# Optimization experiments

Measured on AMD Instinct MI355X. Metric: run time of the kernel, lower is better.

## Reference

```python
import jax, jax.numpy as jnp
import numpy as np

TRANSLATE_STD = 0.125
SCALE_STD = 0.2
CUTOUT_SIZE = 0.5

B, C, H, W = 64, 3, 512, 512


def setup_inputs() -> dict:
    key = jax.random.key(0)
    ks = jax.random.split(key, 20)
    inp = {
        'images': jax.random.normal(ks[0], (B, C, H, W), dtype=jnp.float32),
        'u_angle': jax.random.uniform(ks[1], (B,), dtype=jnp.float32),
        'u_scale': jax.random.uniform(ks[2], (B,), dtype=jnp.float32),
        'u_trans': jax.random.uniform(ks[3], (B,), dtype=jnp.float32),
        'u_bright': jax.random.uniform(ks[4], (B,), dtype=jnp.float32),
        'u_contrast': jax.random.uniform(ks[5], (B,), dtype=jnp.float32),
        'u_sat': jax.random.uniform(ks[6], (B,), dtype=jnp.float32),
        'noise': jax.random.normal(ks[7], (B, C, H, W), dtype=jnp.float32),
        'm_flip': jax.random.randint(ks[8], (B,), 0, 2, dtype=jnp.int32),
        'm_rot': jax.random.randint(ks[9], (B,), 0, 2, dtype=jnp.int32),
        'm_scale': jax.random.randint(ks[10], (B,), 0, 2, dtype=jnp.int32),
        'm_trans': jax.random.randint(ks[11], (B,), 0, 2, dtype=jnp.int32),
        'm_bright': jax.random.randint(ks[12], (B,), 0, 2, dtype=jnp.int32),
        'm_contrast': jax.random.randint(ks[13], (B,), 0, 2, dtype=jnp.int32),
        'm_sat': jax.random.randint(ks[14], (B,), 0, 2, dtype=jnp.int32),
        'm_cut': jax.random.randint(ks[15], (B,), 0, 2, dtype=jnp.int32),
        'y0': jax.random.randint(ks[16], (B,), 0, H - int(H * CUTOUT_SIZE) + 1, dtype=jnp.int32),
        'x0': jax.random.randint(ks[17], (B,), 0, W - int(W * CUTOUT_SIZE) + 1, dtype=jnp.int32),
    }
    return inp


def _sample_bilinear_reflect(img, gx, gy):
    # img: [C,H,W]; gx, gy: [H,W] normalized coords in grid_sample convention
    # (align_corners=False, padding_mode='reflection')
    c, h, w = img.shape
    x = ((gx + 1.0) * w - 1.0) * 0.5
    y = ((gy + 1.0) * h - 1.0) * 0.5

    def reflect(v, size):
        # reflect about pixel edges [-0.5, size-0.5], then clip coordinate
        v = jnp.abs(v + 0.5)
        v = jnp.mod(v, 2.0 * size)
        v = jnp.minimum(v, 2.0 * size - v)
        return jnp.clip(v - 0.5, 0.0, size - 1.0)

    x = reflect(x, float(w))
    y = reflect(y, float(h))
    x0f = jnp.floor(x)
    y0f = jnp.floor(y)
    wx = x - x0f
    wy = y - y0f
    x0i = jnp.clip(x0f, 0, w - 1).astype(jnp.int32)
    x1i = jnp.clip(x0f + 1, 0, w - 1).astype(jnp.int32)
    y0i = jnp.clip(y0f, 0, h - 1).astype(jnp.int32)
    y1i = jnp.clip(y0f + 1, 0, h - 1).astype(jnp.int32)
    v00 = img[:, y0i, x0i]
    v01 = img[:, y0i, x1i]
    v10 = img[:, y1i, x0i]
    v11 = img[:, y1i, x1i]
    top = v00 + wx * (v01 - v00)
    bot = v10 + wx * (v11 - v10)
    return top + wy * (bot - top)


def reference(images, u_angle, u_scale, u_trans, u_bright, u_contrast, u_sat,
              noise, m_flip, m_rot, m_scale, m_trans, m_bright, m_contrast,
              m_sat, m_cut, y0, x0):
    b, c, h, w = images.shape
    # xflip
    images = jnp.where((m_flip > 0)[:, None, None, None], images[..., ::-1], images)
    # rotate / scale / translate (single value broadcast to both axes, as in original)
    angle = jnp.where(m_rot > 0, (u_angle * 2.0 - 1.0) * jnp.pi, 0.0)
    sc = jnp.where(m_scale > 0, (u_scale * 2.0 - 1.0) * SCALE_STD + 1.0, 1.0)
    tr = jnp.where(m_trans > 0, (u_trans * 2.0 - 1.0) * TRANSLATE_STD, 0.0)
    ca = jnp.cos(angle)[:, None, None]
    sa = jnp.sin(angle)[:, None, None]
    scb = sc[:, None, None]
    trb = tr[:, None, None]
    gx0, gy0 = jnp.meshgrid(jnp.linspace(-1.0, 1.0, w), jnp.linspace(-1.0, 1.0, h), indexing='xy')  # [H,W]
    gx = scb * (ca * gx0 - sa * gy0) + trb  # [B,H,W]
    gy = scb * (sa * gx0 + ca * gy0) + trb
    images = jax.vmap(_sample_bilinear_reflect)(images, gx, gy)
    # brightness
    bb = jnp.where(m_bright > 0, u_bright * 0.2, 0.0)
    images = jnp.clip(images + bb[:, None, None, None], -1.0, 1.0)
    # contrast
    cc = jnp.where(m_contrast > 0, u_contrast + 0.5, 1.0)
    images = jnp.clip(images * cc[:, None, None, None], -1.0, 1.0)
    # saturation: lerp(grayscale, images, s)
    ss = jnp.where(m_sat > 0, u_sat * 2.0, 1.0)[:, None, None, None]
    gray = images.mean(axis=1, keepdims=True)
    images = jnp.clip(gray + ss * (images - gray), -1.0, 1.0)
    ch, cw = int(h * CUTOUT_SIZE), int(w * CUTOUT_SIZE)
    ys = jnp.arange(h)[None, :, None]
    xs = jnp.arange(w)[None, None, :]
    y0b = y0[:, None, None]
    x0b = x0[:, None, None]
    cmask = (ys >= y0b) & (ys < y0b + ch) & (xs >= x0b) & (xs < x0b + cw)
    fmask = cmask & (m_cut > 0)[:, None, None]
    images = jnp.where(fmask[:, None, :, :], noise, images)
    return images
```

## Files before the change

kernel.cpp:

```cpp
#include <hip/hip_runtime.h>
#include <math.h>


constexpr int Bn = 64;
constexpr int Cn = 3;
constexpr int Hn = 512;
constexpr int Wn = 512;
constexpr float TRANSLATE_STD = 0.125f;
constexpr float SCALE_STD = 0.2f;
constexpr int CUT_H = 256;
constexpr int CUT_W = 256;

typedef float f2v __attribute__((ext_vector_type(2)));

__device__ __forceinline__ f2v load2(const float* p) {
    f2v r;
    __builtin_memcpy(&r, p, 8);
    return r;
}

__device__ __forceinline__ float reflect_coord(float v, float size) {
    v = fabsf(v + 0.5f);
    v = fmodf(v, 2.0f * size);
    v = fminf(v, 2.0f * size - v);
    return fminf(fmaxf(v - 0.5f, 0.0f), size - 1.0f);
}

__global__ __launch_bounds__(256) void augment_kernel(
    const float* __restrict__ images,
    const float* __restrict__ u_angle,
    const float* __restrict__ u_scale,
    const float* __restrict__ u_trans,
    const float* __restrict__ u_bright,
    const float* __restrict__ u_contrast,
    const float* __restrict__ u_sat,
    const float* __restrict__ noise,
    const int* __restrict__ m_flip,
    const int* __restrict__ m_rot,
    const int* __restrict__ m_scale,
    const int* __restrict__ m_trans,
    const int* __restrict__ m_bright,
    const int* __restrict__ m_contrast,
    const int* __restrict__ m_sat,
    const int* __restrict__ m_cut,
    const int* __restrict__ y0p,
    const int* __restrict__ x0p,
    float* __restrict__ out)
{
    const int x = blockIdx.x * 32 + threadIdx.x;
    const int y = blockIdx.y * 8 + threadIdx.y;
    const int b = blockIdx.z;

    const float angle = (m_rot[b] > 0) ? (u_angle[b] * 2.0f - 1.0f) * 3.14159265358979323846f : 0.0f;
    const float sc    = (m_scale[b] > 0) ? (u_scale[b] * 2.0f - 1.0f) * SCALE_STD + 1.0f : 1.0f;
    const float tr    = (m_trans[b] > 0) ? (u_trans[b] * 2.0f - 1.0f) * TRANSLATE_STD : 0.0f;
    const float bb    = (m_bright[b] > 0) ? u_bright[b] * 0.2f : 0.0f;
    const float cc    = (m_contrast[b] > 0) ? u_contrast[b] + 0.5f : 1.0f;
    const float ss    = (m_sat[b] > 0) ? u_sat[b] * 2.0f : 1.0f;
    const bool  flip  = m_flip[b] > 0;
    const bool  docut = m_cut[b] > 0;
    const int   cy0   = y0p[b];
    const int   cx0   = x0p[b];

    float saf, caf;
    __sincosf(angle, &saf, &caf);

    const float gx0 = -1.0f + (2.0f / 511.0f) * (float)x;
    const float gy0 = -1.0f + (2.0f / 511.0f) * (float)y;

    const float gx = sc * (caf * gx0 - saf * gy0) + tr;
    const float gy = sc * (saf * gx0 + caf * gy0) + tr;

    float xx = ((gx + 1.0f) * (float)Wn - 1.0f) * 0.5f;
    float yy = ((gy + 1.0f) * (float)Hn - 1.0f) * 0.5f;
    xx = reflect_coord(xx, (float)Wn);
    yy = reflect_coord(yy, (float)Hn);

    const float x0f = floorf(xx);
    const float y0f = floorf(yy);
    const float wx = xx - x0f;
    const float wy = yy - y0f;

    int x0i = (int)fminf(fmaxf(x0f, 0.0f), (float)(Wn - 1));
    int x1i = (int)fminf(x0f + 1.0f, (float)(Wn - 1));
    const int y0i = (int)fminf(fmaxf(y0f, 0.0f), (float)(Hn - 1));
    const int y1i = (int)fminf(y0f + 1.0f, (float)(Hn - 1));

    if (flip) { x0i = (Wn - 1) - x0i; x1i = (Wn - 1) - x1i; }

    const int xbase = min(min(x0i, x1i), Wn - 2);
    const bool s0 = (x0i != xbase);
    const bool s1 = (x1i != xbase);

    const size_t plane = (size_t)Hn * Wn;
    const float* imgb = images + (size_t)b * Cn * plane;
    const int r0 = y0i * Wn + xbase;
    const int r1 = y1i * Wn + xbase;

    float vals[Cn];
    #pragma unroll
    for (int c = 0; c < Cn; ++c) {
        const float* p = imgb + (size_t)c * plane;
        const f2v t0 = load2(p + r0);
        const f2v t1 = load2(p + r1);
        const float v00 = s0 ? t0.y : t0.x;
        const float v01 = s1 ? t0.y : t0.x;
        const float v10 = s0 ? t1.y : t1.x;
        const float v11 = s1 ? t1.y : t1.x;
        const float top = v00 + wx * (v01 - v00);
        const float bot = v10 + wx * (v11 - v10);
        float v = top + wy * (bot - top);
        v = fminf(fmaxf(v + bb, -1.0f), 1.0f);
        v = fminf(fmaxf(v * cc, -1.0f), 1.0f);
        vals[c] = v;
    }

    const float gray = (vals[0] + vals[1] + vals[2]) * (1.0f / 3.0f);
    const bool cut = docut && (y >= cy0) && (y < cy0 + CUT_H) && (x >= cx0) && (x < cx0 + CUT_W);

    const size_t base = (size_t)b * Cn * plane + (size_t)y * Wn + (size_t)x;
    #pragma unroll
    for (int c = 0; c < Cn; ++c) {
        float v = gray + ss * (vals[c] - gray);
        v = fminf(fmaxf(v, -1.0f), 1.0f);
        if (cut) v = __builtin_nontemporal_load(&noise[base + c * plane]);
        __builtin_nontemporal_store(v, &out[base + c * plane]);
    }
}

extern "C" void kernel_launch(void* const* d_in, const int* in_sizes, int n_in,
                              void* d_out, int out_size, void* d_ws, size_t ws_size,
                              hipStream_t stream) {
    const float* images     = (const float*)d_in[0];
    const float* u_angle    = (const float*)d_in[1];
    const float* u_scale    = (const float*)d_in[2];
    const float* u_trans    = (const float*)d_in[3];
    const float* u_bright   = (const float*)d_in[4];
    const float* u_contrast = (const float*)d_in[5];
    const float* u_sat      = (const float*)d_in[6];
    const float* noise      = (const float*)d_in[7];
    const int*   m_flip     = (const int*)d_in[8];
    const int*   m_rot      = (const int*)d_in[9];
    const int*   m_scale    = (const int*)d_in[10];
    const int*   m_trans    = (const int*)d_in[11];
    const int*   m_bright   = (const int*)d_in[12];
    const int*   m_contrast = (const int*)d_in[13];
    const int*   m_sat      = (const int*)d_in[14];
    const int*   m_cut      = (const int*)d_in[15];
    const int*   y0p        = (const int*)d_in[16];
    const int*   x0p        = (const int*)d_in[17];
    float* out = (float*)d_out;

    dim3 block(32, 8);
    dim3 grid(Wn / 32, Hn / 8, Bn);
    augment_kernel<<<grid, block, 0, stream>>>(
        images, u_angle, u_scale, u_trans, u_bright, u_contrast, u_sat, noise,
        m_flip, m_rot, m_scale, m_trans, m_bright, m_contrast, m_sat, m_cut,
        y0p, x0p, out);
}
```

Measured before the change: 511.4 us.

## Stage source footprint in LDS per 16x16 tile and loop tiles per block

Each block now handles eight 16x16 output tiles in sequence. For each tile it computes the bounding box of the rotated and scaled source footprint and loads that region into LDS with coalesced float4 loads, flipping in-register when needed. Bilinear taps then read from LDS instead of scattered 8-byte global loads. Tiles whose footprint nears an edge or is too tall (large scale or rotation) fall back to the original reflect path. Coordinates are stepped incrementally and clamps use fmed3. The cost is extra syncs and LDS traffic, plus divergence between the staged and fallback paths.

```diff
diff --git a/kernel.cpp b/kernel.cpp
--- a/kernel.cpp
+++ b/kernel.cpp
@@ -11,6 +11,14 @@
 constexpr int CUT_H = 256;
 constexpr int CUT_W = 256;
 
+constexpr int FW = 32;
+constexpr int FSTRIDE = 40;
+constexpr int FH_MAX = 32;
+constexpr int CH_LDS = FSTRIDE * FH_MAX;
+constexpr int NT = 8;
+constexpr uint32_t PLANE = 512u * 512u;
+
+typedef float f4v __attribute__((ext_vector_type(4)));
 typedef float f2v __attribute__((ext_vector_type(2)));
 
 __device__ __forceinline__ f2v load2(const float* p) {
@@ -47,9 +55,13 @@
     const int* __restrict__ x0p,
     float* __restrict__ out)
 {
-    const int x = blockIdx.x * 32 + threadIdx.x;
-    const int y = blockIdx.y * 8 + threadIdx.y;
-    const int b = blockIdx.z;
+    __shared__ __align__(16) float lds[Cn * CH_LDS];
+
+    const int tx  = threadIdx.x;
+    const int ty  = threadIdx.y;
+    const int sx0 = blockIdx.x * (16 * NT);
+    const int y   = blockIdx.y * 16 + ty;
+    const int b   = blockIdx.z;
 
     const float angle = (m_rot[b] > 0) ? (u_angle[b] * 2.0f - 1.0f) * 3.14159265358979323846f : 0.0f;
     const float sc    = (m_scale[b] > 0) ? (u_scale[b] * 2.0f - 1.0f) * SCALE_STD + 1.0f : 1.0f;
@@ -65,66 +77,142 @@
     float saf, caf;
     __sincosf(angle, &saf, &caf);
 
-    const float gx0 = -1.0f + (2.0f / 511.0f) * (float)x;
-    const float gy0 = -1.0f + (2.0f / 511.0f) * (float)y;
-
-    const float gx = sc * (caf * gx0 - saf * gy0) + tr;
-    const float gy = sc * (saf * gx0 + caf * gy0) + tr;
-
-    float xx = ((gx + 1.0f) * (float)Wn - 1.0f) * 0.5f;
-    float yy = ((gy + 1.0f) * (float)Hn - 1.0f) * 0.5f;
-    xx = reflect_coord(xx, (float)Wn);
-    yy = reflect_coord(yy, (float)Hn);
-
-    const float x0f = floorf(xx);
-    const float y0f = floorf(yy);
-    const float wx = xx - x0f;
-    const float wy = yy - y0f;
-
-    int x0i = (int)fminf(fmaxf(x0f, 0.0f), (float)(Wn - 1));
-    int x1i = (int)fminf(x0f + 1.0f, (float)(Wn - 1));
-    const int y0i = (int)fminf(fmaxf(y0f, 0.0f), (float)(Hn - 1));
-    const int y1i = (int)fminf(y0f + 1.0f, (float)(Hn - 1));
-
-    if (flip) { x0i = (Wn - 1) - x0i; x1i = (Wn - 1) - x1i; }
-
-    const int xbase = min(min(x0i, x1i), Wn - 2);
-    const bool s0 = (x0i != xbase);
-    const bool s1 = (x1i != xbase);
-
-    const size_t plane = (size_t)Hn * Wn;
-    const float* imgb = images + (size_t)b * Cn * plane;
-    const int r0 = y0i * Wn + xbase;
-    const int r1 = y1i * Wn + xbase;
-
-    float vals[Cn];
-    #pragma unroll
-    for (int c = 0; c < Cn; ++c) {
-        const float* p = imgb + (size_t)c * plane;
-        const f2v t0 = load2(p + r0);
-        const f2v t1 = load2(p + r1);
-        const float v00 = s0 ? t0.y : t0.x;
-        const float v01 = s1 ? t0.y : t0.x;
-        const float v10 = s0 ? t1.y : t1.x;
-        const float v11 = s1 ? t1.y : t1.x;
-        const float top = v00 + wx * (v01 - v00);
-        const float bot = v10 + wx * (v11 - v10);
-        float v = top + wy * (bot - top);
-        v = fminf(fmaxf(v + bb, -1.0f), 1.0f);
-        v = fminf(fmaxf(v * cc, -1.0f), 1.0f);
-        vals[c] = v;
-    }
-
-    const float gray = (vals[0] + vals[1] + vals[2]) * (1.0f / 3.0f);
-    const bool cut = docut && (y >= cy0) && (y < cy0 + CUT_H) && (x >= cx0) && (x < cx0 + CUT_W);
-
-    const size_t base = (size_t)b * Cn * plane + (size_t)y * Wn + (size_t)x;
-    #pragma unroll
-    for (int c = 0; c < Cn; ++c) {
-        float v = gray + ss * (vals[c] - gray);
-        v = fminf(fmaxf(v, -1.0f), 1.0f);
-        if (cut) v = __builtin_nontemporal_load(&noise[base + c * plane]);
-        __builtin_nontemporal_store(v, &out[base + c * plane]);
+    const float kk = sc * (512.0f / 511.0f);
+    const float dxdx = caf * kk, dxdy = -saf * kk;
+    const float dydx = saf * kk, dydy = caf * kk;
+    const float xx_org = 256.0f * (sc * (saf - caf) + tr + 1.0f) - 0.5f;
+    const float yy_org = 256.0f * (sc * (-saf - caf) + tr + 1.0f) - 0.5f;
+
+    const float step_x = 16.0f * dxdx;
+    const float step_y = 16.0f * dydx;
+
+    float xxt = xx_org + (float)(sx0 + tx) * dxdx + (float)y * dxdy;
+    float yyt = yy_org + (float)(sx0 + tx) * dydx + (float)y * dydy;
+
+    const float fty = (float)(blockIdx.y * 16);
+    float bx = xx_org + (float)sx0 * dxdx + fty * dxdy;
+    float by = yy_org + (float)sx0 * dydx + fty * dydy;
+    const float sxx = 15.0f * dxdx, sxy = 15.0f * dxdy;
+    const float syx = 15.0f * dydx, syy = 15.0f * dydy;
+    const float min_dx = fminf(sxx, 0.0f) + fminf(sxy, 0.0f);
+    const float max_dx = fmaxf(sxx, 0.0f) + fmaxf(sxy, 0.0f);
+    const float min_dy = fminf(syx, 0.0f) + fminf(syy, 0.0f);
+    const float max_dy = fmaxf(syx, 0.0f) + fmaxf(syy, 0.0f);
+
+    const float* __restrict__ imgb = images + (size_t)b * (Cn * PLANE);
+    float* __restrict__ outb       = out    + (size_t)b * (Cn * PLANE);
+    const float* __restrict__ noib = noise  + (size_t)b * (Cn * PLANE);
+
+    const int tid = ty * 16 + tx;
+    const int sr  = tid >> 3;
+    const int sq  = (tid & 7) << 2;
+
+    const bool ycut = docut && (y >= cy0) && (y < cy0 + CUT_H);
+    uint32_t opix = (uint32_t)y * 512u + (uint32_t)(sx0 + tx);
+
+    #pragma unroll 1
+    for (int t = 0; t < NT; ++t) {
+        const float minxx = bx + min_dx, maxxx = bx + max_dx;
+        const float minyy = by + min_dy, maxyy = by + max_dy;
+        bool cok = (minxx >= 1.0f) && (maxxx <= 509.0f) &&
+                   (minyy >= 1.0f) && (maxyy <= 509.0f);
+        int x_lo = 0, y_lo = 0, fh = 0;
+        if (cok) {
+            x_lo = min(((int)minxx - 1) & ~3, Wn - FW);
+            y_lo = (int)minyy - 1;
+            fh   = ((int)maxyy + 2) - y_lo + 1;
+            if (fh > FH_MAX) cok = false;
+        }
+
+        if (t > 0) __syncthreads();
+
+        if (cok && sr < fh) {
+            const int scol = flip ? (508 - x_lo - sq) : (x_lo + sq);
+            const uint32_t soff = (uint32_t)(y_lo + sr) * 512u + (uint32_t)scol;
+            f4v A = *(const f4v*)(imgb + soff);
+            f4v B = *(const f4v*)(imgb + soff + PLANE);
+            f4v C = *(const f4v*)(imgb + soff + 2 * PLANE);
+            if (flip) {
+                A = f4v{A.w, A.z, A.y, A.x};
+                B = f4v{B.w, B.z, B.y, B.x};
+                C = f4v{C.w, C.z, C.y, C.x};
+            }
+            float* d = &lds[sr * FSTRIDE + sq];
+            *(f4v*)(d)              = A;
+            *(f4v*)(d + CH_LDS)     = B;
+            *(f4v*)(d + 2 * CH_LDS) = C;
+        }
+        __syncthreads();
+
+        float vals[Cn];
+        if (cok) {
+            const float fx = xxt - (float)x_lo;
+            const float fy = yyt - (float)y_lo;
+            const int xi = (int)fx;
+            const int yi = (int)fy;
+            const float wx = fx - (float)xi;
+            const float wy = fy - (float)yi;
+            const float* ph = &lds[yi * FSTRIDE + xi];
+            #pragma unroll
+            for (int c = 0; c < Cn; ++c) {
+                const float v00 = ph[0], v01 = ph[1];
+                const float v10 = ph[FSTRIDE], v11 = ph[FSTRIDE + 1];
+                ph += CH_LDS;
+                const float top = v00 + wx * (v01 - v00);
+                const float bot = v10 + wx * (v11 - v10);
+                float v = top + wy * (bot - top);
+                v = __builtin_amdgcn_fmed3f(v + bb, -1.0f, 1.0f);
+                v = __builtin_amdgcn_fmed3f(v * cc, -1.0f, 1.0f);
+                vals[c] = v;
+            }
+        } else {
+            const float rxx = reflect_coord(xxt, (float)Wn);
+            const float ryy = reflect_coord(yyt, (float)Hn);
+            const float x0f = floorf(rxx);
+            const float y0f = floorf(ryy);
+            const float wx = rxx - x0f;
+            const float wy = ryy - y0f;
+            int x0i = (int)fminf(fmaxf(x0f, 0.0f), 511.0f);
+            int x1i = (int)fminf(x0f + 1.0f, 511.0f);
+            const int y0i = (int)fminf(fmaxf(y0f, 0.0f), 511.0f);
+            const int y1i = (int)fminf(y0f + 1.0f, 511.0f);
+            if (flip) { x0i = 511 - x0i; x1i = 511 - x1i; }
+            const int xbase = min(min(x0i, x1i), 510);
+            const bool s0 = (x0i != xbase);
+            const bool s1 = (x1i != xbase);
+            const uint32_t r0 = (uint32_t)(y0i * 512 + xbase);
+            const uint32_t r1 = (uint32_t)(y1i * 512 + xbase);
+            #pragma unroll
+            for (int c = 0; c < Cn; ++c) {
+                const f2v t0 = load2(imgb + r0 + c * PLANE);
+                const f2v t1 = load2(imgb + r1 + c * PLANE);
+                const float v00 = s0 ? t0.y : t0.x;
+                const float v01 = s1 ? t0.y : t0.x;
+                const float v10 = s0 ? t1.y : t1.x;
+                const float v11 = s1 ? t1.y : t1.x;
+                const float top = v00 + wx * (v01 - v00);
+                const float bot = v10 + wx * (v11 - v10);
+                float v = top + wy * (bot - top);
+                v = __builtin_amdgcn_fmed3f(v + bb, -1.0f, 1.0f);
+                v = __builtin_amdgcn_fmed3f(v * cc, -1.0f, 1.0f);
+                vals[c] = v;
+            }
+        }
+
+        const float gray = (vals[0] + vals[1] + vals[2]) * (1.0f / 3.0f);
+        const int xpix = sx0 + (t << 4) + tx;
+        const bool cut = ycut && (xpix >= cx0) && (xpix < cx0 + CUT_W);
+        #pragma unroll
+        for (int c = 0; c < Cn; ++c) {
+            float v = gray + ss * (vals[c] - gray);
+            v = __builtin_amdgcn_fmed3f(v, -1.0f, 1.0f);
+            if (cut) v = __builtin_nontemporal_load(&noib[opix + c * PLANE]);
+            __builtin_nontemporal_store(v, &outb[opix + c * PLANE]);
+        }
+
+        opix += 16;
+        bx += step_x; by += step_y;
+        xxt += step_x; yyt += step_y;
     }
 }
 
@@ -151,8 +239,8 @@
     const int*   x0p        = (const int*)d_in[17];
     float* out = (float*)d_out;
 
-    dim3 block(32, 8);
-    dim3 grid(Wn / 32, Hn / 8, Bn);
+    dim3 block(16, 16);
+    dim3 grid(Wn / (16 * NT), Hn / 16, Bn);
     augment_kernel<<<grid, block, 0, stream>>>(
         images, u_angle, u_scale, u_trans, u_bright, u_contrast, u_sat, noise,
         m_flip, m_rot, m_scale, m_trans, m_bright, m_contrast, m_sat, m_cut,
```

After: 517.8 us. Within noise of the previous version (+1.3%).
